# Optimization experiments

Hardware: AMD Instinct MI355X
Metric: run time of the kernel (lower is better)

## Reference

```python
import jax, jax.numpy as jnp
import numpy as np

N = 100000      # vertices
E = 1600000     # edges of the hypergraph-derived graph (avg degree 16)
CIN = 128
COUT = 64


def setup_inputs() -> dict:
    key = jax.random.key(0)
    k1, k2, k3, k4 = jax.random.split(key, 4)
    X = jax.random.normal(k1, (N, CIN), dtype=jnp.float32)
    # theta Linear params (nn.Linear(in, out)): W stored as (CIN, COUT) for x @ W
    W = jax.random.normal(k2, (CIN, COUT), dtype=jnp.float32) / np.sqrt(CIN)
    b = jnp.zeros((COUT,), dtype=jnp.float32)
    src = jax.random.randint(k3, (E,), 0, N, dtype=jnp.int32)
    dst = jax.random.randint(k4, (E,), 0, N, dtype=jnp.int32)
    return {"X": X, "W": W, "b": b, "src": src, "dst": dst}


def reference(X, W, b, src, dst):
    # theta: (N, CIN) -> (N, COUT)
    H = X @ W + b
    n = H.shape[0]
    ones = jnp.ones(src.shape[0], dtype=H.dtype)
    # GCN normalization with self-loops: d_i = 1 + deg_i
    deg = jax.ops.segment_sum(ones, dst, num_segments=n)
    dinv_sqrt = jax.lax.rsqrt(1.0 + deg)          # (N,)
    # edge messages: D^{-1/2}[src] * D^{-1/2}[dst] * H[src], scattered to dst
    coef = dinv_sqrt[src] * dinv_sqrt[dst]        # (E,)
    msg = H[src] * coef[:, None]                  # (E, COUT) gather
    agg = jax.ops.segment_sum(msg, dst, num_segments=n)  # (N, COUT) scatter-add
    # self-loop term: D^{-1/2} I D^{-1/2} H = H / d
    out = agg + H * (dinv_sqrt * dinv_sqrt)[:, None]
    # is_last=False, use_bn=False: ReLU; dropout is identity in eval mode
    return jax.nn.relu(out)
```

## Files before the change

### kernel.cpp

```cpp
#include <hip/hip_runtime.h>

#define CIN 128
#define COUT 64
#define NBSH 8
#define NBK_MAX 512
#define CHUNK 4096
#define BMAX 8192

typedef unsigned int u32;
typedef unsigned short u16;
typedef __attribute__((ext_vector_type(8))) __bf16 bf16x8;
typedef __attribute__((ext_vector_type(4))) float f32x4;

union B8 { u32 u[4]; uint4 q; bf16x8 v; };

__device__ __forceinline__ u16 bf16rne(float x) {
    u32 u = __float_as_uint(x);
    u += 0x7fffu + ((u >> 16) & 1u);
    return (u16)(u >> 16);
}


__global__ void zero_i32_kernel(int* __restrict__ p, int n) {
    int i = blockIdx.x * blockDim.x + threadIdx.x;
    int stride = gridDim.x * blockDim.x;
    for (; i < n; i += stride) p[i] = 0;
}


__global__ __launch_bounds__(256) void bcount_kernel(
    const int* __restrict__ dst, int* __restrict__ bcount, int E, int nbk) {
    __shared__ int hist[NBK_MAX];
    const int t = threadIdx.x;
    const int e0 = blockIdx.x * CHUNK;
    const int e1 = (e0 + CHUNK < E) ? e0 + CHUNK : E;
    for (int i = t; i < nbk; i += 256) hist[i] = 0;
    __syncthreads();
    for (int i = e0 + t; i < e1; i += 256) atomicAdd(&hist[dst[i] >> NBSH], 1);
    __syncthreads();
    for (int i = t; i < nbk; i += 256) {
        int c = hist[i];
        if (c) atomicAdd(&bcount[i], c);
    }
}


__global__ __launch_bounds__(512) void bscan_kernel(
    const int* __restrict__ bcount, int* __restrict__ bbase,
    int* __restrict__ bcursor, int nbk, int E) {
    __shared__ int sh[NBK_MAX];
    const int t = threadIdx.x;
    int v = (t < nbk) ? bcount[t] : 0;
    sh[t] = v;
    __syncthreads();
    #pragma unroll
    for (int ofs = 1; ofs < NBK_MAX; ofs <<= 1) {
        int u = (t >= ofs) ? sh[t - ofs] : 0;
        __syncthreads();
        sh[t] += u;
        __syncthreads();
    }
    int excl = sh[t] - v;
    if (t < nbk) { bbase[t] = excl; bcursor[t] = excl; }
    if (t == 0) bbase[nbk] = E;
}


__global__ __launch_bounds__(256) void bucket_kernel(
    const int* __restrict__ src, const int* __restrict__ dst,
    int* __restrict__ bcursor, int* __restrict__ esrc, int E, int nbk) {
    __shared__ int hist[NBK_MAX];
    __shared__ int base[NBK_MAX];
    const int t = threadIdx.x;
    const int e0 = blockIdx.x * CHUNK;
    const int e1 = (e0 + CHUNK < E) ? e0 + CHUNK : E;

    for (int i = t; i < nbk; i += 256) hist[i] = 0;
    __syncthreads();
    for (int i = e0 + t; i < e1; i += 256) atomicAdd(&hist[dst[i] >> NBSH], 1);
    __syncthreads();
    for (int i = t; i < nbk; i += 256) {
        int c = hist[i];
        base[i] = c ? atomicAdd(&bcursor[i], c) : 0;
        hist[i] = 0;
    }
    __syncthreads();
    for (int i = e0 + t; i < e1; i += 256) {
        int d = dst[i];
        int b = d >> NBSH;
        int pos = base[b] + atomicAdd(&hist[b], 1);
        esrc[pos] = (src[i] << NBSH) | (d & ((1 << NBSH) - 1));
    }
}


__global__ __launch_bounds__(256) void place2_kernel(
    const int* __restrict__ bbase, int* __restrict__ esrc,
    int* __restrict__ deg, float* __restrict__ dinv, int* __restrict__ offs, int n) {
    __shared__ int stage[BMAX];
    __shared__ int hist[1 << NBSH];
    __shared__ int lofs[1 << NBSH];
    __shared__ int scn[1 << NBSH];
    __shared__ int lcur[1 << NBSH];
    const int b = blockIdx.x;
    const int t = threadIdx.x;
    const int gbase = bbase[b];
    int cnt = bbase[b + 1] - gbase;
    if (cnt > BMAX) cnt = BMAX;

    hist[t] = 0;
    lcur[t] = 0;
    for (int i = t; i < cnt; i += 256) stage[i] = esrc[gbase + i];
    __syncthreads();
    for (int i = t; i < cnt; i += 256) atomicAdd(&hist[stage[i] & ((1 << NBSH) - 1)], 1);
    __syncthreads();

    int myv = hist[t];
    scn[t] = myv;
    __syncthreads();
    #pragma unroll
    for (int ofs = 1; ofs < 256; ofs <<= 1) {
        int u = (t >= ofs) ? scn[t - ofs] : 0;
        __syncthreads();
        scn[t] += u;
        __syncthreads();
    }
    int excl = scn[t] - myv;
    lofs[t] = excl;

    const int v = (b << NBSH) + t;
    if (v < n) {
        deg[v] = myv;
        dinv[v] = rsqrtf(1.0f + (float)myv);
        offs[v] = gbase + excl;
    }
    __syncthreads();

    for (int i = t; i < cnt; i += 256) {
        int e = stage[i];
        int l = e & ((1 << NBSH) - 1);
        int pos = gbase + lofs[l] + atomicAdd(&lcur[l], 1);
        esrc[pos] = e >> NBSH;
    }
}


__global__ __launch_bounds__(256) void gemm_kernel(
    const float* __restrict__ X, const float* __restrict__ W,
    const float* __restrict__ bias, const float* __restrict__ dinv,
    u16* __restrict__ Hs, int n) {
    __shared__ __align__(16) u16 Wt[64 * 128];
    const int t = threadIdx.x;
    const int lane = t & 63;
    const int q = lane >> 4;
    const int cl = lane & 15;
    const int row0 = blockIdx.x * 128 + (t >> 6) * 32;

    for (int i = t; i < CIN * COUT; i += 256) {
        int k = i >> 6, c = i & 63;
        int byte = (c << 8) + (k << 1);
        byte ^= (c & 7) << 4;
        *(u16*)((char*)Wt + byte) = bf16rne(W[i]);
    }
    __syncthreads();

    f32x4 acc[2][4];
    #pragma unroll
    for (int mt = 0; mt < 2; ++mt)
        #pragma unroll
        for (int nt = 0; nt < 4; ++nt)
            acc[mt][nt] = (f32x4){0.0f, 0.0f, 0.0f, 0.0f};

    #pragma unroll
    for (int kk = 0; kk < 4; ++kk) {
        bf16x8 a[2], bfr[4];
        #pragma unroll
        for (int mt = 0; mt < 2; ++mt) {
            int row = row0 + mt * 16 + cl;
            const float* xp = X + (size_t)(row < n ? row : 0) * CIN + kk * 32 + q * 8;
            float4 x0 = *(const float4*)xp;
            float4 x1 = *(const float4*)(xp + 4);
            B8 pk;
            pk.u[0] = (u32)bf16rne(x0.x) | ((u32)bf16rne(x0.y) << 16);
            pk.u[1] = (u32)bf16rne(x0.z) | ((u32)bf16rne(x0.w) << 16);
            pk.u[2] = (u32)bf16rne(x1.x) | ((u32)bf16rne(x1.y) << 16);
            pk.u[3] = (u32)bf16rne(x1.z) | ((u32)bf16rne(x1.w) << 16);
            a[mt] = pk.v;
        }
        #pragma unroll
        for (int nt = 0; nt < 4; ++nt) {
            int c = nt * 16 + cl;
            int byte = (c << 8) + ((kk * 32 + q * 8) << 1);
            byte ^= (c & 7) << 4;
            B8 pk;
            pk.q = *(const uint4*)((const char*)Wt + byte);
            bfr[nt] = pk.v;
        }
        #pragma unroll
        for (int mt = 0; mt < 2; ++mt)
            #pragma unroll
            for (int nt = 0; nt < 4; ++nt)
                acc[mt][nt] = __builtin_amdgcn_mfma_f32_16x16x32_bf16(
                    a[mt], bfr[nt], acc[mt][nt], 0, 0, 0);
    }

    #pragma unroll
    for (int mt = 0; mt < 2; ++mt) {
        const int rbase = row0 + mt * 16 + q * 4;
        float dv[4];
        #pragma unroll
        for (int r = 0; r < 4; ++r)
            dv[r] = (rbase + r < n) ? dinv[rbase + r] : 0.0f;
        #pragma unroll
        for (int nt = 0; nt < 4; ++nt) {
            const int col = nt * 16 + cl;
            const float bc = bias[col];
            #pragma unroll
            for (int r = 0; r < 4; ++r) {
                int row = rbase + r;
                if (row < n)
                    Hs[(size_t)row * COUT + col] = bf16rne((acc[mt][nt][r] + bc) * dv[r]);
            }
        }
    }
}


__global__ __launch_bounds__(256) void gather_kernel(
    const u16* __restrict__ Hs, const int* __restrict__ esrc,
    const int* __restrict__ offs, const int* __restrict__ deg,
    const float* __restrict__ dinv, float* __restrict__ out, int n) {
    const int wave = (blockIdx.x * blockDim.x + threadIdx.x) >> 6;
    const int lane = threadIdx.x & 63;
    if (wave >= n) return;
    const int v = wave;
    const int slot = lane >> 4;
    const int cg = lane & 15;

    float a0 = 0.0f, a1 = 0.0f, a2 = 0.0f, a3 = 0.0f;
    const int off = offs[v];
    const int d = deg[v];

    for (int j0 = 0; j0 < d; j0 += 64) {
        int my = j0 + lane;
        int s_l = (my < d) ? esrc[off + my] : 0;
        int m = (d - j0 < 64) ? (d - j0) : 64;
        for (int j = 0; j < m; j += 4) {
            int s = __shfl(s_l, j + slot);
            if (j + slot < m) {
                uint2 h = *(const uint2*)&Hs[(size_t)s * COUT + cg * 4];
                a0 += __uint_as_float(h.x << 16);
                a1 += __uint_as_float(h.x & 0xffff0000u);
                a2 += __uint_as_float(h.y << 16);
                a3 += __uint_as_float(h.y & 0xffff0000u);
            }
        }
    }
    a0 += __shfl_xor(a0, 16); a1 += __shfl_xor(a1, 16);
    a2 += __shfl_xor(a2, 16); a3 += __shfl_xor(a3, 16);
    a0 += __shfl_xor(a0, 32); a1 += __shfl_xor(a1, 32);
    a2 += __shfl_xor(a2, 32); a3 += __shfl_xor(a3, 32);

    if (slot == 0) {
        uint2 h = *(const uint2*)&Hs[(size_t)v * COUT + cg * 4];
        a0 += __uint_as_float(h.x << 16);
        a1 += __uint_as_float(h.x & 0xffff0000u);
        a2 += __uint_as_float(h.y << 16);
        a3 += __uint_as_float(h.y & 0xffff0000u);
        float dv = dinv[v];
        float4 o;
        o.x = fmaxf(a0 * dv, 0.0f);
        o.y = fmaxf(a1 * dv, 0.0f);
        o.z = fmaxf(a2 * dv, 0.0f);
        o.w = fmaxf(a3 * dv, 0.0f);
        *(float4*)&out[(size_t)v * COUT + cg * 4] = o;
    }
}

extern "C" void kernel_launch(void* const* d_in, const int* in_sizes, int n_in,
                              void* d_out, int out_size, void* d_ws, size_t ws_size,
                              hipStream_t stream) {
    const float* X    = (const float*)d_in[0];
    const float* W    = (const float*)d_in[1];
    const float* bias = (const float*)d_in[2];
    const int*   src  = (const int*)d_in[3];
    const int*   dst  = (const int*)d_in[4];
    float* out = (float*)d_out;

    const int n = in_sizes[0] / CIN;
    const int E = in_sizes[3];
    const int nbk = (n + (1 << NBSH) - 1) >> NBSH;
    const int nchunk = (E + CHUNK - 1) / CHUNK;

    char* ws = (char*)d_ws;
    size_t o = 0;
    u16*   Hs      = (u16*)(ws + o);   o += (size_t)n * COUT * 2;
    int*   esrc    = (int*)(ws + o);   o += (size_t)E * 4;
    int*   deg     = (int*)(ws + o);   o += (size_t)n * 4;
    int*   offs    = (int*)(ws + o);   o += (size_t)n * 4;
    float* dinv    = (float*)(ws + o); o += (size_t)n * 4;
    int*   bcount  = (int*)(ws + o);   o += NBK_MAX * 4;
    int*   bbase   = (int*)(ws + o);   o += (NBK_MAX + 1) * 4;
    int*   bcursor = (int*)(ws + o);   o += NBK_MAX * 4;

    zero_i32_kernel<<<1, 512, 0, stream>>>(bcount, NBK_MAX);
    bcount_kernel<<<nchunk, 256, 0, stream>>>(dst, bcount, E, nbk);
    bscan_kernel<<<1, 512, 0, stream>>>(bcount, bbase, bcursor, nbk, E);
    bucket_kernel<<<nchunk, 256, 0, stream>>>(src, dst, bcursor, esrc, E, nbk);
    place2_kernel<<<nbk, 256, 0, stream>>>(bbase, esrc, deg, dinv, offs, n);
    gemm_kernel<<<(n + 127) / 128, 256, 0, stream>>>(X, W, bias, dinv, Hs, n);
    gather_kernel<<<(n * 64 + 255) / 256, 256, 0, stream>>>(
        Hs, esrc, offs, deg, dinv, out, n);
}
```

Before: 217.8 us.

## Replace global-atomic bucket sort with per-chunk local sort and column scans

The edge bucketing pipeline is restructured. Instead of a global histogram pass followed by a scatter through global atomic cursors, each chunk now sorts its edges locally in shared memory and writes per-chunk counts and offsets. A column scan and a bucket scan derive the placement, and place2 gathers each bucket's runs from every chunk. This removes the separate count pass over dst and the global atomics, at the cost of an extra temporary buffer and short serial per-thread copy loops in place2. Nontemporal loads and stores are also added to the gemm, gather and bucketing kernels.

```diff
diff --git a/kernel.cpp b/kernel.cpp
--- a/kernel.cpp
+++ b/kernel.cpp
@@ -3,9 +3,9 @@
 #define CIN 128
 #define COUT 64
 #define NBSH 8
-#define NBK_MAX 512
+#define CS 512
 #define CHUNK 4096
-#define BMAX 8192
+#define BMAX 5120
 
 typedef unsigned int u32;
 typedef unsigned short u16;
@@ -21,104 +21,151 @@
 }
 
 
-__global__ void zero_i32_kernel(int* __restrict__ p, int n) {
-    int i = blockIdx.x * blockDim.x + threadIdx.x;
-    int stride = gridDim.x * blockDim.x;
-    for (; i < n; i += stride) p[i] = 0;
-}
-
-
-__global__ __launch_bounds__(256) void bcount_kernel(
-    const int* __restrict__ dst, int* __restrict__ bcount, int E, int nbk) {
-    __shared__ int hist[NBK_MAX];
-    const int t = threadIdx.x;
-    const int e0 = blockIdx.x * CHUNK;
-    const int e1 = (e0 + CHUNK < E) ? e0 + CHUNK : E;
-    for (int i = t; i < nbk; i += 256) hist[i] = 0;
-    __syncthreads();
-    for (int i = e0 + t; i < e1; i += 256) atomicAdd(&hist[dst[i] >> NBSH], 1);
-    __syncthreads();
-    for (int i = t; i < nbk; i += 256) {
-        int c = hist[i];
-        if (c) atomicAdd(&bcount[i], c);
-    }
-}
-
-
-__global__ __launch_bounds__(512) void bscan_kernel(
-    const int* __restrict__ bcount, int* __restrict__ bbase,
-    int* __restrict__ bcursor, int nbk, int E) {
-    __shared__ int sh[NBK_MAX];
-    const int t = threadIdx.x;
-    int v = (t < nbk) ? bcount[t] : 0;
-    sh[t] = v;
-    __syncthreads();
-    #pragma unroll
-    for (int ofs = 1; ofs < NBK_MAX; ofs <<= 1) {
-        int u = (t >= ofs) ? sh[t - ofs] : 0;
-        __syncthreads();
-        sh[t] += u;
-        __syncthreads();
-    }
-    int excl = sh[t] - v;
-    if (t < nbk) { bbase[t] = excl; bcursor[t] = excl; }
-    if (t == 0) bbase[nbk] = E;
-}
-
-
-__global__ __launch_bounds__(256) void bucket_kernel(
+__global__ __launch_bounds__(512) void bucket_local_kernel(
     const int* __restrict__ src, const int* __restrict__ dst,
-    int* __restrict__ bcursor, int* __restrict__ esrc, int E, int nbk) {
-    __shared__ int hist[NBK_MAX];
-    __shared__ int base[NBK_MAX];
-    const int t = threadIdx.x;
-    const int e0 = blockIdx.x * CHUNK;
-    const int e1 = (e0 + CHUNK < E) ? e0 + CHUNK : E;
-
-    for (int i = t; i < nbk; i += 256) hist[i] = 0;
-    __syncthreads();
-    for (int i = e0 + t; i < e1; i += 256) atomicAdd(&hist[dst[i] >> NBSH], 1);
-    __syncthreads();
-    for (int i = t; i < nbk; i += 256) {
-        int c = hist[i];
-        base[i] = c ? atomicAdd(&bcursor[i], c) : 0;
-        hist[i] = 0;
-    }
-    __syncthreads();
-    for (int i = e0 + t; i < e1; i += 256) {
-        int d = dst[i];
-        int b = d >> NBSH;
-        int pos = base[b] + atomicAdd(&hist[b], 1);
-        esrc[pos] = (src[i] << NBSH) | (d & ((1 << NBSH) - 1));
-    }
-}
-
-
-__global__ __launch_bounds__(256) void place2_kernel(
-    const int* __restrict__ bbase, int* __restrict__ esrc,
-    int* __restrict__ deg, float* __restrict__ dinv, int* __restrict__ offs, int n) {
-    __shared__ int stage[BMAX];
-    __shared__ int hist[1 << NBSH];
-    __shared__ int lofs[1 << NBSH];
-    __shared__ int scn[1 << NBSH];
-    __shared__ int lcur[1 << NBSH];
-    const int b = blockIdx.x;
-    const int t = threadIdx.x;
-    const int gbase = bbase[b];
-    int cnt = bbase[b + 1] - gbase;
-    if (cnt > BMAX) cnt = BMAX;
-
-    hist[t] = 0;
-    lcur[t] = 0;
-    for (int i = t; i < cnt; i += 256) stage[i] = esrc[gbase + i];
-    __syncthreads();
-    for (int i = t; i < cnt; i += 256) atomicAdd(&hist[stage[i] & ((1 << NBSH) - 1)], 1);
+    int* __restrict__ tmp, int* __restrict__ cnt, int* __restrict__ rowoff,
+    int E) {
+    __shared__ int hist[CS];
+    __shared__ int scn[CS];
+    __shared__ int lofs[CS];
+    __shared__ int lcur[CS];
+    __shared__ int stage[CHUNK];
+    const int t = threadIdx.x;
+    const int c = blockIdx.x;
+    const int e0 = c * CHUNK;
+    const int m = (E - e0 < CHUNK) ? (E - e0) : CHUNK;
+
+    hist[t] = 0; lcur[t] = 0;
+    __syncthreads();
+
+    int pk[8], bb[8];
+    #pragma unroll
+    for (int j = 0; j < 8; ++j) {
+        int i = t + j * 512;
+        bool ok = i < m;
+        int d = ok ? __builtin_nontemporal_load(&dst[e0 + i]) : 0;
+        int s = ok ? __builtin_nontemporal_load(&src[e0 + i]) : 0;
+        pk[j] = (s << NBSH) | (d & ((1 << NBSH) - 1));
+        bb[j] = d >> NBSH;
+        if (ok) atomicAdd(&hist[bb[j]], 1);
+    }
     __syncthreads();
 
     int myv = hist[t];
     scn[t] = myv;
     __syncthreads();
     #pragma unroll
+    for (int ofs = 1; ofs < CS; ofs <<= 1) {
+        int u = (t >= ofs) ? scn[t - ofs] : 0;
+        __syncthreads();
+        scn[t] += u;
+        __syncthreads();
+    }
+    lofs[t] = scn[t] - myv;
+    cnt[c * CS + t] = myv;
+    rowoff[c * CS + t] = scn[t] - myv;
+    __syncthreads();
+
+    #pragma unroll
+    for (int j = 0; j < 8; ++j) {
+        int i = t + j * 512;
+        if (i < m) {
+            int b = bb[j];
+            int pos = lofs[b] + atomicAdd(&lcur[b], 1);
+            stage[pos] = pk[j];
+        }
+    }
+    __syncthreads();
+    for (int i = t; i < m; i += 512) tmp[e0 + i] = stage[i];
+}
+
+
+__global__ __launch_bounds__(512) void colscan_kernel(
+    const int* __restrict__ cnt, int* __restrict__ coloffT,
+    int* __restrict__ cntT, int* __restrict__ btot, int nchunk) {
+    __shared__ int sh[CS];
+    const int t = threadIdx.x;
+    const int k = blockIdx.x;
+    int v = (t < nchunk) ? cnt[t * CS + k] : 0;
+    sh[t] = v;
+    __syncthreads();
+    #pragma unroll
+    for (int ofs = 1; ofs < CS; ofs <<= 1) {
+        int u = (t >= ofs) ? sh[t - ofs] : 0;
+        __syncthreads();
+        sh[t] += u;
+        __syncthreads();
+    }
+    coloffT[k * CS + t] = sh[t] - v;
+    cntT[k * CS + t] = v;
+    if (t == CS - 1) btot[k] = sh[t];
+}
+
+
+__global__ __launch_bounds__(512) void bscan_kernel(
+    const int* __restrict__ btot, int* __restrict__ bbase, int nbk, int E) {
+    __shared__ int sh[CS];
+    const int t = threadIdx.x;
+    int v = (t < nbk) ? btot[t] : 0;
+    sh[t] = v;
+    __syncthreads();
+    #pragma unroll
+    for (int ofs = 1; ofs < CS; ofs <<= 1) {
+        int u = (t >= ofs) ? sh[t - ofs] : 0;
+        __syncthreads();
+        sh[t] += u;
+        __syncthreads();
+    }
+    if (t < nbk) bbase[t] = sh[t] - v;
+    if (t == 0) bbase[nbk] = E;
+}
+
+
+__global__ __launch_bounds__(256) void place2_kernel(
+    const int* __restrict__ tmp, const int* __restrict__ cntT,
+    const int* __restrict__ coloffT, const int* __restrict__ rowoff,
+    const int* __restrict__ bbase, int* __restrict__ esrc,
+    int* __restrict__ deg, float* __restrict__ dinv, int* __restrict__ offs,
+    int n, int nchunk) {
+    __shared__ int stage[BMAX];
+    __shared__ int coloffs[CS];
+    __shared__ int cnts[CS];
+    __shared__ int rowoffs[CS];
+    __shared__ int hist[1 << NBSH];
+    __shared__ int scn[1 << NBSH];
+    __shared__ int lofs[1 << NBSH];
+    __shared__ int lcur[1 << NBSH];
+    const int k = blockIdx.x;
+    const int t = threadIdx.x;
+
+    for (int i = t; i < CS; i += 256) {
+        coloffs[i] = coloffT[k * CS + i];
+        cnts[i] = cntT[k * CS + i];
+        rowoffs[i] = (i < nchunk) ? rowoff[i * CS + k] : 0;
+    }
+    hist[t] = 0; lcur[t] = 0;
+    __syncthreads();
+
+    const int gbase = bbase[k];
+    int total = bbase[k + 1] - gbase;
+    if (total > BMAX) total = BMAX;
+
+    for (int c = t; c < nchunk; c += 256) {
+        int rc = cnts[c];
+        int sb = c * CHUNK + rowoffs[c];
+        int db = coloffs[c];
+        for (int j = 0; j < rc; ++j) stage[db + j] = tmp[sb + j];
+    }
+    __syncthreads();
+
+    for (int i = t; i < total; i += 256)
+        atomicAdd(&hist[stage[i] & ((1 << NBSH) - 1)], 1);
+    __syncthreads();
+
+    int myv = hist[t];
+    scn[t] = myv;
+    __syncthreads();
+    #pragma unroll
     for (int ofs = 1; ofs < 256; ofs <<= 1) {
         int u = (t >= ofs) ? scn[t - ofs] : 0;
         __syncthreads();
@@ -128,7 +175,7 @@
     int excl = scn[t] - myv;
     lofs[t] = excl;
 
-    const int v = (b << NBSH) + t;
+    const int v = (k << NBSH) + t;
     if (v < n) {
         deg[v] = myv;
         dinv[v] = rsqrtf(1.0f + (float)myv);
@@ -136,7 +183,7 @@
     }
     __syncthreads();
 
-    for (int i = t; i < cnt; i += 256) {
+    for (int i = t; i < total; i += 256) {
         int e = stage[i];
         int l = e & ((1 << NBSH) - 1);
         int pos = gbase + lofs[l] + atomicAdd(&lcur[l], 1);
@@ -178,13 +225,13 @@
         for (int mt = 0; mt < 2; ++mt) {
             int row = row0 + mt * 16 + cl;
             const float* xp = X + (size_t)(row < n ? row : 0) * CIN + kk * 32 + q * 8;
-            float4 x0 = *(const float4*)xp;
-            float4 x1 = *(const float4*)(xp + 4);
+            f32x4 x0 = __builtin_nontemporal_load((const f32x4*)xp);
+            f32x4 x1 = __builtin_nontemporal_load((const f32x4*)(xp + 4));
             B8 pk;
-            pk.u[0] = (u32)bf16rne(x0.x) | ((u32)bf16rne(x0.y) << 16);
-            pk.u[1] = (u32)bf16rne(x0.z) | ((u32)bf16rne(x0.w) << 16);
-            pk.u[2] = (u32)bf16rne(x1.x) | ((u32)bf16rne(x1.y) << 16);
-            pk.u[3] = (u32)bf16rne(x1.z) | ((u32)bf16rne(x1.w) << 16);
+            pk.u[0] = (u32)bf16rne(x0[0]) | ((u32)bf16rne(x0[1]) << 16);
+            pk.u[1] = (u32)bf16rne(x0[2]) | ((u32)bf16rne(x0[3]) << 16);
+            pk.u[2] = (u32)bf16rne(x1[0]) | ((u32)bf16rne(x1[1]) << 16);
+            pk.u[3] = (u32)bf16rne(x1[2]) | ((u32)bf16rne(x1[3]) << 16);
             a[mt] = pk.v;
         }
         #pragma unroll
@@ -243,7 +290,7 @@
 
     for (int j0 = 0; j0 < d; j0 += 64) {
         int my = j0 + lane;
-        int s_l = (my < d) ? esrc[off + my] : 0;
+        int s_l = (my < d) ? __builtin_nontemporal_load(&esrc[off + my]) : 0;
         int m = (d - j0 < 64) ? (d - j0) : 64;
         for (int j = 0; j < m; j += 4) {
             int s = __shfl(s_l, j + slot);
@@ -268,12 +315,12 @@
         a2 += __uint_as_float(h.y << 16);
         a3 += __uint_as_float(h.y & 0xffff0000u);
         float dv = dinv[v];
-        float4 o;
-        o.x = fmaxf(a0 * dv, 0.0f);
-        o.y = fmaxf(a1 * dv, 0.0f);
-        o.z = fmaxf(a2 * dv, 0.0f);
-        o.w = fmaxf(a3 * dv, 0.0f);
-        *(float4*)&out[(size_t)v * COUT + cg * 4] = o;
+        f32x4 o;
+        o[0] = fmaxf(a0 * dv, 0.0f);
+        o[1] = fmaxf(a1 * dv, 0.0f);
+        o[2] = fmaxf(a2 * dv, 0.0f);
+        o[3] = fmaxf(a3 * dv, 0.0f);
+        __builtin_nontemporal_store(o, (f32x4*)&out[(size_t)v * COUT + cg * 4]);
     }
 }
 
@@ -296,18 +343,22 @@
     size_t o = 0;
     u16*   Hs      = (u16*)(ws + o);   o += (size_t)n * COUT * 2;
     int*   esrc    = (int*)(ws + o);   o += (size_t)E * 4;
+    int*   tmp     = (int*)(ws + o);   o += (size_t)nchunk * CHUNK * 4;
+    int*   cnt     = (int*)(ws + o);   o += (size_t)nchunk * CS * 4;
+    int*   rowoff  = (int*)(ws + o);   o += (size_t)nchunk * CS * 4;
+    int*   cntT    = (int*)(ws + o);   o += (size_t)nbk * CS * 4;
+    int*   coloffT = (int*)(ws + o);   o += (size_t)nbk * CS * 4;
     int*   deg     = (int*)(ws + o);   o += (size_t)n * 4;
     int*   offs    = (int*)(ws + o);   o += (size_t)n * 4;
     float* dinv    = (float*)(ws + o); o += (size_t)n * 4;
-    int*   bcount  = (int*)(ws + o);   o += NBK_MAX * 4;
-    int*   bbase   = (int*)(ws + o);   o += (NBK_MAX + 1) * 4;
-    int*   bcursor = (int*)(ws + o);   o += NBK_MAX * 4;
-
-    zero_i32_kernel<<<1, 512, 0, stream>>>(bcount, NBK_MAX);
-    bcount_kernel<<<nchunk, 256, 0, stream>>>(dst, bcount, E, nbk);
-    bscan_kernel<<<1, 512, 0, stream>>>(bcount, bbase, bcursor, nbk, E);
-    bucket_kernel<<<nchunk, 256, 0, stream>>>(src, dst, bcursor, esrc, E, nbk);
-    place2_kernel<<<nbk, 256, 0, stream>>>(bbase, esrc, deg, dinv, offs, n);
+    int*   btot    = (int*)(ws + o);   o += CS * 4;
+    int*   bbase   = (int*)(ws + o);   o += (CS + 1) * 4;
+
+    bucket_local_kernel<<<nchunk, 512, 0, stream>>>(src, dst, tmp, cnt, rowoff, E);
+    colscan_kernel<<<nbk, 512, 0, stream>>>(cnt, coloffT, cntT, btot, nchunk);
+    bscan_kernel<<<1, 512, 0, stream>>>(btot, bbase, nbk, E);
+    place2_kernel<<<nbk, 256, 0, stream>>>(tmp, cntT, coloffT, rowoff, bbase,
+                                           esrc, deg, dinv, offs, n, nchunk);
     gemm_kernel<<<(n + 127) / 128, 256, 0, stream>>>(X, W, bias, dinv, Hs, n);
     gather_kernel<<<(n * 64 + 255) / 256, 256, 0, stream>>>(
         Hs, esrc, offs, deg, dinv, out, n);
```

Result: faster. 209.7 us (-3.7%).
